# Performance work log

Measured on AMD Instinct MI355X. Metric: run time of the kernel, lower is better.

Reference implementation:

```python
import jax, jax.numpy as jnp
from jax import lax
import numpy as np

THRESH = 0.5
R = 4  # suppression radius -> (2R+1)^3 max-pool window


def setup_inputs() -> dict:
    key = jax.random.key(0)
    pred_vol = jax.random.uniform(key, (1, 1, 64, 512, 512), dtype=jnp.float32)
    return {"pred_vol": pred_vol}


def reference(pred_vol):
    # Threshold: keep values above thresh, zero otherwise
    pred_thresh = jnp.where(pred_vol > THRESH, pred_vol, jnp.float32(0.0))
    # 3D max-pool, kernel 2R+1, stride 1, padding R (pad with -inf so padding
    k = 2 * R + 1
    conf = lax.reduce_window(
        pred_thresh,
        -jnp.inf,
        lax.max,
        window_dimensions=(1, 1, k, k, k),
        window_strides=(1, 1, 1, 1, 1),
        padding=[(0, 0), (0, 0), (R, R), (R, R), (R, R)],
    )
    # Keep only strict local maxima of the thresholded volume
    conf = jnp.where((conf > 0.0) & (conf == pred_thresh), conf, jnp.float32(0.0))
    return jnp.squeeze(conf)  # [D, H, W]
```

## Files before the change

kernel.cpp:

```cpp
#include <hip/hip_runtime.h>

static constexpr int Dd = 64;
static constexpr int Hh = 512;
static constexpr int Ww = 512;
static constexpr int RAD = 4;
static constexpr float THRESH_V = 0.5f;
static constexpr int W4 = Ww / 4;
static constexpr int PLANE4 = Hh * W4;

static constexpr int TH = 4;
static constexpr int DC = 16;
static constexpr int ROWS = TH + 2 * RAD;
static constexpr int NPL = DC + 2 * RAD;
static constexpr int NBLK = (Hh / TH) * (Dd / DC);

typedef float nf4 __attribute__((ext_vector_type(4)));

__device__ __forceinline__ float4 f4max(float4 a, float4 b) {
    return make_float4(fmaxf(a.x, b.x), fmaxf(a.y, b.y), fmaxf(a.z, b.z), fmaxf(a.w, b.w));
}
__device__ __forceinline__ int iclamp(int v, int lo, int hi) {
    return v < lo ? lo : (v > hi ? hi : v);
}

static constexpr int DPP_WAVE_SHR1 = 0x138;
static constexpr int DPP_WAVE_SHL1 = 0x130;
template <int CTRL>
__device__ __forceinline__ float4 f4dpp(float4 v) {
    float4 r;
    r.x = __int_as_float(__builtin_amdgcn_update_dpp(
        __float_as_int(v.x), __float_as_int(v.x), CTRL, 0xF, 0xF, false));
    r.y = __int_as_float(__builtin_amdgcn_update_dpp(
        __float_as_int(v.y), __float_as_int(v.y), CTRL, 0xF, 0xF, false));
    r.z = __int_as_float(__builtin_amdgcn_update_dpp(
        __float_as_int(v.z), __float_as_int(v.z), CTRL, 0xF, 0xF, false));
    r.w = __int_as_float(__builtin_amdgcn_update_dpp(
        __float_as_int(v.w), __float_as_int(v.w), CTRL, 0xF, 0xF, false));
    return r;
}

#define BAR_VM(N) asm volatile("s_waitcnt vmcnt(" #N ") lgkmcnt(0)\n\ts_barrier" ::: "memory")
#define BAR_LDS() asm volatile("s_waitcnt lgkmcnt(0)\n\ts_barrier" ::: "memory")

__device__ __forceinline__ void load_lds16(const float4* g, float4* l) {
    __builtin_amdgcn_global_load_lds(
        (const __attribute__((address_space(1))) void*)g,
        (__attribute__((address_space(3))) void*)l, 16, 0, 0);
}

__global__ __launch_bounds__(512, 2)
void fused_nms_k9(const float4* __restrict__ x4, float4* __restrict__ o4) {
    __shared__ float4 braw[3][ROWS * W4];
    __shared__ float4 bpatch[2][TH][2];

    const int tid  = threadIdx.x;
    const int w4   = tid & (W4 - 1);
    const int hr   = tid >> 7;
    const int wid  = tid >> 6;
    const int lane = tid & 63;

    const int b    = blockIdx.x;
    const int band = b & 7;
    const int rest = b >> 3;
    const int ht   = band * 16 + (rest & 15);
    const int dc   = rest >> 4;
    const int h0   = ht * TH;
    const int d0   = dc * DC;
    const int outrow = (h0 + hr) * W4 + w4;

    int goff[3], loff[3];
#pragma unroll
    for (int k = 0; k < 3; ++k) {
        const int s    = wid + 8 * k;
        const int row  = s >> 1;
        const int half = s & 1;
        const int gh   = iclamp(h0 - RAD + row, 0, Hh - 1);
        goff[k] = gh * W4 + half * 64 + lane;
        loff[k] = row * W4 + half * 64;
    }

    auto stage = [&](int p) {
        const int gd = iclamp(d0 - RAD + p, 0, Dd - 1);
        const float4* pl = x4 + (size_t)gd * PLANE4;
        float4* dst = braw[p % 3];
#pragma unroll
        for (int k = 0; k < 3; ++k)
            load_lds16(pl + goff[k], dst + loff[k]);
    };

    float4 R[8];
    float4 C[5];
    float4 vp;

    stage(0);
    stage(1);

#pragma unroll
    for (int t = 0; t <= NPL; ++t) {
        const bool doV = (t <= NPL - 1);
        const bool doH = (t >= 1);
        const bool doE = (t >= 9);

        if (t <= 9)       { BAR_VM(3); }
        else if (t == 10) { BAR_VM(4); }
        else if (t <= 22) { BAR_VM(5); }
        else if (t == 23) { BAR_VM(2); }
        else              { BAR_LDS(); }

        if (t + 2 <= NPL - 1) stage(t + 2);
        __builtin_amdgcn_sched_barrier(0);

        float4 nv, nc;
        if (doV) {
            const float4* Bc = &braw[t % 3][tid];
            float4 r0 = Bc[0 * W4], r1 = Bc[1 * W4], r2 = Bc[2 * W4], r3 = Bc[3 * W4];
            float4 r4 = Bc[4 * W4];
            float4 r5 = Bc[5 * W4], r6 = Bc[6 * W4], r7 = Bc[7 * W4], r8 = Bc[8 * W4];
            nv = f4max(f4max(f4max(r0, r1), f4max(r2, r3)),
                       f4max(f4max(r4, r5), f4max(f4max(r6, r7), r8)));
            nc = r4;
            if (w4 == 63) bpatch[t & 1][hr][0] = nv;
            if (w4 == 64) bpatch[t & 1][hr][1] = nv;
        }

        if (doH) {
            const int p1 = (t - 1) & 1;
            float4 lm = f4dpp<DPP_WAVE_SHR1>(vp);
            float4 rm = f4dpp<DPP_WAVE_SHL1>(vp);
            if (w4 == 64) lm = bpatch[p1][hr][0];
            if (w4 == 63) rm = bpatch[p1][hr][1];
            const float l3 = lm.w, l2 = fmaxf(lm.z, l3), l1 = fmaxf(lm.y, l2), l0 = fmaxf(lm.x, l1);
            const float core = fmaxf(fmaxf(vp.x, vp.y), fmaxf(vp.z, vp.w));
            const float q0 = rm.x, q1 = fmaxf(q0, rm.y), q2 = fmaxf(q1, rm.z), q3 = fmaxf(q2, rm.w);
            float4 pm;
            pm.x = fmaxf(l0, fmaxf(core, q0));
            pm.y = fmaxf(l1, fmaxf(core, q1));
            pm.z = fmaxf(l2, fmaxf(core, q2));
            pm.w = fmaxf(l3, fmaxf(core, q3));

            if (doE) {
                const float4 cen = C[t % 5];
                float4 mm = pm;
#pragma unroll
                for (int i = 0; i < 8; ++i) mm = f4max(mm, R[i]);
                nf4 q;
                q.x = (cen.x > THRESH_V && cen.x == mm.x) ? cen.x : 0.0f;
                q.y = (cen.y > THRESH_V && cen.y == mm.y) ? cen.y : 0.0f;
                q.z = (cen.z > THRESH_V && cen.z == mm.z) ? cen.z : 0.0f;
                q.w = (cen.w > THRESH_V && cen.w == mm.w) ? cen.w : 0.0f;
                __builtin_nontemporal_store(
                    q, (nf4*)&o4[(size_t)(d0 + t - 9) * PLANE4 + outrow]);
            }
            R[(t - 1) & 7] = pm;
        }

        if (doV) {
            vp = nv;
            C[t % 5] = nc;
        }
    }
}

extern "C" void kernel_launch(void* const* d_in, const int* in_sizes, int n_in,
                              void* d_out, int out_size, void* d_ws, size_t ws_size,
                              hipStream_t stream) {
    const float4* x4 = (const float4*)d_in[0];
    float4* out4 = (float4*)d_out;
    (void)d_ws; (void)ws_size; (void)in_sizes; (void)n_in; (void)out_size;
    fused_nms_k9<<<dim3(NBLK), dim3(512), 0, stream>>>(x4, out4);
}
```

Baseline: 124.9 us.

## Double row tile to 8 with 1024-thread blocks and LDS-based horizontal neighbor exchange

Raises the H tile from 4 to 8 rows per block, launching 1024 threads per block, so the 8-row vertical halo is amortized over more output rows and global/LDS traffic per output drops. The horizontal neighbor exchange moves from DPP wave shifts plus boundary patches to a full LDS column buffer that every thread writes and then reads at its left and right neighbors. This costs extra LDS capacity and traffic and lowers occupancy to one block per CU. The wait counts are retuned for two loads per stage instead of three.

```diff
diff --git a/kernel.cpp b/kernel.cpp
--- a/kernel.cpp
+++ b/kernel.cpp
@@ -8,7 +8,7 @@
 static constexpr int W4 = Ww / 4;
 static constexpr int PLANE4 = Hh * W4;
 
-static constexpr int TH = 4;
+static constexpr int TH = 8;
 static constexpr int DC = 16;
 static constexpr int ROWS = TH + 2 * RAD;
 static constexpr int NPL = DC + 2 * RAD;
@@ -23,22 +23,6 @@
     return v < lo ? lo : (v > hi ? hi : v);
 }
 
-static constexpr int DPP_WAVE_SHR1 = 0x138;
-static constexpr int DPP_WAVE_SHL1 = 0x130;
-template <int CTRL>
-__device__ __forceinline__ float4 f4dpp(float4 v) {
-    float4 r;
-    r.x = __int_as_float(__builtin_amdgcn_update_dpp(
-        __float_as_int(v.x), __float_as_int(v.x), CTRL, 0xF, 0xF, false));
-    r.y = __int_as_float(__builtin_amdgcn_update_dpp(
-        __float_as_int(v.y), __float_as_int(v.y), CTRL, 0xF, 0xF, false));
-    r.z = __int_as_float(__builtin_amdgcn_update_dpp(
-        __float_as_int(v.z), __float_as_int(v.z), CTRL, 0xF, 0xF, false));
-    r.w = __int_as_float(__builtin_amdgcn_update_dpp(
-        __float_as_int(v.w), __float_as_int(v.w), CTRL, 0xF, 0xF, false));
-    return r;
-}
-
 #define BAR_VM(N) asm volatile("s_waitcnt vmcnt(" #N ") lgkmcnt(0)\n\ts_barrier" ::: "memory")
 #define BAR_LDS() asm volatile("s_waitcnt lgkmcnt(0)\n\ts_barrier" ::: "memory")
 
@@ -48,10 +32,10 @@
         (__attribute__((address_space(3))) void*)l, 16, 0, 0);
 }
 
-__global__ __launch_bounds__(512, 2)
-void fused_nms_k9(const float4* __restrict__ x4, float4* __restrict__ o4) {
+__global__ __launch_bounds__(1024, 1)
+void fused_nms_k10(const float4* __restrict__ x4, float4* __restrict__ o4) {
     __shared__ float4 braw[3][ROWS * W4];
-    __shared__ float4 bpatch[2][TH][2];
+    __shared__ float4 bcol[2][TH * W4];
 
     const int tid  = threadIdx.x;
     const int w4   = tid & (W4 - 1);
@@ -62,16 +46,19 @@
     const int b    = blockIdx.x;
     const int band = b & 7;
     const int rest = b >> 3;
-    const int ht   = band * 16 + (rest & 15);
-    const int dc   = rest >> 4;
+    const int ht   = band * 8 + (rest & 7);
+    const int dc   = rest >> 3;
     const int h0   = ht * TH;
     const int d0   = dc * DC;
+
+    const int colm = w4 ? w4 - 1 : 0;
+    const int colp = (w4 < W4 - 1) ? w4 + 1 : W4 - 1;
     const int outrow = (h0 + hr) * W4 + w4;
 
-    int goff[3], loff[3];
+    int goff[2], loff[2];
 #pragma unroll
-    for (int k = 0; k < 3; ++k) {
-        const int s    = wid + 8 * k;
+    for (int k = 0; k < 2; ++k) {
+        const int s    = wid + 16 * k;
         const int row  = s >> 1;
         const int half = s & 1;
         const int gh   = iclamp(h0 - RAD + row, 0, Hh - 1);
@@ -83,9 +70,8 @@
         const int gd = iclamp(d0 - RAD + p, 0, Dd - 1);
         const float4* pl = x4 + (size_t)gd * PLANE4;
         float4* dst = braw[p % 3];
-#pragma unroll
-        for (int k = 0; k < 3; ++k)
-            load_lds16(pl + goff[k], dst + loff[k]);
+        load_lds16(pl + goff[0], dst + loff[0]);
+        load_lds16(pl + goff[1], dst + loff[1]);
     };
 
     float4 R[8];
@@ -101,9 +87,9 @@
         const bool doH = (t >= 1);
         const bool doE = (t >= 9);
 
-        if (t <= 9)       { BAR_VM(3); }
-        else if (t == 10) { BAR_VM(4); }
-        else if (t <= 22) { BAR_VM(5); }
+        if (t <= 9)       { BAR_VM(2); }
+        else if (t == 10) { BAR_VM(3); }
+        else if (t <= 22) { BAR_VM(4); }
         else if (t == 23) { BAR_VM(2); }
         else              { BAR_LDS(); }
 
@@ -119,16 +105,13 @@
             nv = f4max(f4max(f4max(r0, r1), f4max(r2, r3)),
                        f4max(f4max(r4, r5), f4max(f4max(r6, r7), r8)));
             nc = r4;
-            if (w4 == 63) bpatch[t & 1][hr][0] = nv;
-            if (w4 == 64) bpatch[t & 1][hr][1] = nv;
+            bcol[t & 1][tid] = nv;
         }
 
         if (doH) {
-            const int p1 = (t - 1) & 1;
-            float4 lm = f4dpp<DPP_WAVE_SHR1>(vp);
-            float4 rm = f4dpp<DPP_WAVE_SHL1>(vp);
-            if (w4 == 64) lm = bpatch[p1][hr][0];
-            if (w4 == 63) rm = bpatch[p1][hr][1];
+            const float4* Bp = &bcol[(t - 1) & 1][hr * W4];
+            const float4 lm = Bp[colm];
+            const float4 rm = Bp[colp];
             const float l3 = lm.w, l2 = fmaxf(lm.z, l3), l1 = fmaxf(lm.y, l2), l0 = fmaxf(lm.x, l1);
             const float core = fmaxf(fmaxf(vp.x, vp.y), fmaxf(vp.z, vp.w));
             const float q0 = rm.x, q1 = fmaxf(q0, rm.y), q2 = fmaxf(q1, rm.z), q3 = fmaxf(q2, rm.w);
@@ -167,5 +150,5 @@
     const float4* x4 = (const float4*)d_in[0];
     float4* out4 = (float4*)d_out;
     (void)d_ws; (void)ws_size; (void)in_sizes; (void)n_in; (void)out_size;
-    fused_nms_k9<<<dim3(NBLK), dim3(512), 0, stream>>>(x4, out4);
+    fused_nms_k10<<<dim3(NBLK), dim3(1024), 0, stream>>>(x4, out4);
 }
```

Result: faster. 116.0 us (-7.1%).
